# Performance work log

Hardware: AMD Instinct MI355X
Metric: run time of the kernel (lower is better)

The kernel has to match this reference:

```python
import jax, jax.numpy as jnp
import numpy as np

N_NODES = 100000
N_EDGES = 1600000
D = 64
BN_EPS = 1e-5


def setup_inputs() -> dict:
    key = jax.random.key(0)
    ks = jax.random.split(key, 10)
    s = 1.0 / np.sqrt(D)
    return {
        "features": jax.random.normal(ks[0], (N_NODES, D), dtype=jnp.float32),
        "src": jax.random.randint(ks[1], (N_EDGES,), 0, N_NODES, dtype=jnp.int32),
        "dst": jax.random.randint(ks[2], (N_EDGES,), 0, N_NODES, dtype=jnp.int32),
        "eps": jnp.zeros((), dtype=jnp.float32),
        "W1": jax.random.uniform(ks[3], (D, D), jnp.float32, -s, s),
        "b1": jax.random.uniform(ks[4], (D,), jnp.float32, -s, s),
        "W2": jax.random.uniform(ks[5], (D, D), jnp.float32, -s, s),
        "b2": jax.random.uniform(ks[6], (D,), jnp.float32, -s, s),
        "gamma": jnp.ones((D,), dtype=jnp.float32),
        "beta": jnp.zeros((D,), dtype=jnp.float32),
    }


def reference(features, src, dst, eps, W1, b1, W2, b2, gamma, beta):
    h_in = features
    # message passing: gather src node features, scatter-sum to dst (fn.copy_u + fn.sum)
    neigh = jax.ops.segment_sum(features[src], dst, num_segments=N_NODES)  # [N, D]
    # eps-weighted self term
    h = (1.0 + eps) * features + neigh
    # apply_func MLP: Linear -> ReLU -> Linear
    h = jnp.maximum(h @ W1 + b1, 0.0) @ W2 + b2
    # BatchNorm1d over nodes (training-mode batch statistics)
    mean = jnp.mean(h, axis=0)
    var = jnp.var(h, axis=0)
    h = (h - mean) * jax.lax.rsqrt(var + BN_EPS) * gamma + beta
    # activation
    h = jnp.maximum(h, 0.0)
    # residual (indim == outdim)
    h = h_in + h
    # dropout p=0 -> identity
    return h
```

## Files before the change

### kernel.cpp

```cpp
#include <hip/hip_runtime.h>
#include <hip/hip_fp16.h>

#define N_NODES 100000
#define N_EDGES 1600000
#define D 64
#define BN_EPS 1e-5f
#define NSHARD 8

#define NBKT 256
#define NPB 391
#define BKT_CAP 8192
#define NBBLK 391
#define SORT_T 1024

typedef _Float16 half8 __attribute__((ext_vector_type(8)));
typedef float f32x4 __attribute__((ext_vector_type(4)));

__global__ __launch_bounds__(256) void prep_k(
    const int* __restrict__ src, const int* __restrict__ dst,
    int* __restrict__ bkt_cnt, int* __restrict__ bktbuf,
    const float* __restrict__ feat, __half* __restrict__ feat16,
    const float* __restrict__ W1, const float* __restrict__ W2,
    _Float16* __restrict__ w1t, _Float16* __restrict__ w2t)
{
    __shared__ int h[NBKT], base[NBKT], cur[NBKT];
    const int blk = blockIdx.x;
    const int t = threadIdx.x;

    if (blk < NBBLK) {
        h[t] = 0; cur[t] = 0;
        __syncthreads();
        const int e0 = blk * 4096;
        int pk[16], b[16];
        #pragma unroll
        for (int i = 0; i < 16; ++i) {
            int e = e0 + i * 256 + t;
            if (e < N_EDGES) {
                int d = dst[e];
                b[i] = d / NPB;
                pk[i] = (src[e] << 9) | (d - b[i] * NPB);
                atomicAdd(&h[b[i]], 1);
            } else {
                b[i] = -1;
            }
        }
        __syncthreads();
        base[t] = atomicAdd(&bkt_cnt[t], h[t]);
        __syncthreads();
        #pragma unroll
        for (int i = 0; i < 16; ++i) {
            if (b[i] >= 0) {
                int p = atomicAdd(&cur[b[i]], 1);
                bktbuf[(size_t)b[i] * BKT_CAP + base[b[i]] + p] = pk[i];
            }
        }
    } else if (blk < NBBLK + 3125) {
        size_t i = ((size_t)(blk - NBBLK) * 256 + t) * 8;
        if (i < (size_t)N_NODES * D) {
            float4 v0 = *(const float4*)(feat + i);
            float4 v1 = *(const float4*)(feat + i + 4);
            __half2 o[4];
            o[0] = __floats2half2_rn(v0.x, v0.y);
            o[1] = __floats2half2_rn(v0.z, v0.w);
            o[2] = __floats2half2_rn(v1.x, v1.y);
            o[3] = __floats2half2_rn(v1.z, v1.w);
            *(float4*)(feat16 + i) = *(float4*)o;
        }
    } else {
        const int n = t >> 2;
        const int k0 = (t & 3) * 16;
        _Float16 o1[16], o2[16];
        #pragma unroll
        for (int j = 0; j < 16; ++j) {
            o1[j] = (_Float16)W1[(k0 + j) * 64 + n];
            o2[j] = (_Float16)W2[(k0 + j) * 64 + n];
        }
        #pragma unroll
        for (int j = 0; j < 16; j += 8) {
            *(half8*)(w1t + n * 64 + k0 + j) = *(half8*)&o1[j];
            *(half8*)(w2t + n * 64 + k0 + j) = *(half8*)&o2[j];
        }
    }
}

__global__ __launch_bounds__(SORT_T) void sortp_k(
    const int* __restrict__ bktbuf, const int* __restrict__ bkt_cnt,
    int* __restrict__ rowptr, int* __restrict__ col)
{
    __shared__ int h[NPB];
    __shared__ int cur[NPB];
    __shared__ int part[SORT_T];
    __shared__ int bsc[NBKT];

    const int b = blockIdx.x;
    const int t = threadIdx.x;
    const int nb0 = b * NPB;
    const int nodes_in = min(NPB, N_NODES - nb0);
    const int cnt = min(bkt_cnt[b], BKT_CAP);
    const int* buf = bktbuf + (size_t)b * BKT_CAP;

    if (t < NBKT) bsc[t] = min(bkt_cnt[t], BKT_CAP);
    __syncthreads();
    for (int off = 1; off < NBKT; off <<= 1) {
        int x = 0;
        if (t < NBKT) {
            x = bsc[t];
            if (t >= off) x += bsc[t - off];
        }
        __syncthreads();
        if (t < NBKT) bsc[t] = x;
        __syncthreads();
    }
    const int gbase = bsc[b] - cnt;

    if (t < NPB) h[t] = 0;
    __syncthreads();

    for (int i = t; i < cnt; i += SORT_T)
        atomicAdd(&h[buf[i] & 511], 1);
    __syncthreads();

    int a = (t < NPB) ? h[t] : 0;
    part[t] = a;
    __syncthreads();
    for (int off = 1; off < SORT_T; off <<= 1) {
        int x = part[t];
        int u = (t >= off) ? part[t - off] : 0;
        __syncthreads();
        part[t] = x + u;
        __syncthreads();
    }
    int excl = part[t] - a;
    if (t < NPB) {
        cur[t] = excl;
        if (t < nodes_in) rowptr[nb0 + t] = gbase + excl;
    }
    if (b == NBKT - 1 && t == 0) rowptr[N_NODES] = N_EDGES;
    __syncthreads();

    for (int i = t; i < cnt; i += SORT_T) {
        int pk = buf[i];
        int slot = atomicAdd(&cur[pk & 511], 1);
        col[gbase + slot] = pk >> 9;
    }
}

__device__ __forceinline__ void acc16(float* a, float4 r0, float4 r1)
{
    const __half2* h0 = (const __half2*)&r0;
    const __half2* h1 = (const __half2*)&r1;
    #pragma unroll
    for (int i = 0; i < 4; ++i) {
        float2 f = __half22float2(h0[i]);
        a[2 * i]     += f.x;
        a[2 * i + 1] += f.y;
    }
    #pragma unroll
    for (int i = 0; i < 4; ++i) {
        float2 f = __half22float2(h1[i]);
        a[8 + 2 * i]     += f.x;
        a[8 + 2 * i + 1] += f.y;
    }
}

__global__ __launch_bounds__(256) void gmlp_k(
    const __half* __restrict__ feat16, const int* __restrict__ rowptr,
    const int* __restrict__ col, const float* __restrict__ epsp,
    const _Float16* __restrict__ w1t, const _Float16* __restrict__ w2t,
    const float* __restrict__ b1, const float* __restrict__ b2,
    __half* __restrict__ h216, float* __restrict__ stats)
{
    __shared__ __align__(16) _Float16 xts[64 * 72];

    const int t    = threadIdx.x;
    const int lane = t & 63;
    const int nb   = blockIdx.x * 64;

    {
        const int nl   = t >> 2;
        const int node = nb + nl;
        const int c    = (t & 3) << 4;
        __half2 o[8];

        if (node < N_NODES) {
            const int lo = rowptr[node];
            const int hi = rowptr[node + 1];
            float a[16];
            #pragma unroll
            for (int i = 0; i < 16; ++i) a[i] = 0.f;

            int e = lo;
            for (; e + 3 < hi; e += 4) {
                const int s0 = col[e], s1 = col[e + 1], s2 = col[e + 2], s3 = col[e + 3];
                const __half* p0 = feat16 + (size_t)s0 * 64 + c;
                const __half* p1 = feat16 + (size_t)s1 * 64 + c;
                const __half* p2 = feat16 + (size_t)s2 * 64 + c;
                const __half* p3 = feat16 + (size_t)s3 * 64 + c;
                float4 r00 = *(const float4*)(p0), r01 = *(const float4*)(p0 + 8);
                float4 r10 = *(const float4*)(p1), r11 = *(const float4*)(p1 + 8);
                float4 r20 = *(const float4*)(p2), r21 = *(const float4*)(p2 + 8);
                float4 r30 = *(const float4*)(p3), r31 = *(const float4*)(p3 + 8);
                acc16(a, r00, r01);
                acc16(a, r10, r11);
                acc16(a, r20, r21);
                acc16(a, r30, r31);
            }
            for (; e < hi; ++e) {
                const __half* p = feat16 + (size_t)col[e] * 64 + c;
                float4 r0 = *(const float4*)(p), r1 = *(const float4*)(p + 8);
                acc16(a, r0, r1);
            }

            const float epsv = 1.0f + epsp[0];
            const size_t gb = (size_t)node * 64 + c;
            float4 s0 = *(const float4*)(feat16 + gb);
            float4 s1 = *(const float4*)(feat16 + gb + 8);
            const __half2* h0 = (const __half2*)&s0;
            const __half2* h1 = (const __half2*)&s1;
            #pragma unroll
            for (int i = 0; i < 4; ++i) {
                float2 f = __half22float2(h0[i]);
                o[i] = __floats2half2_rn(fmaf(epsv, f.x, a[2 * i]),
                                         fmaf(epsv, f.y, a[2 * i + 1]));
            }
            #pragma unroll
            for (int i = 0; i < 4; ++i) {
                float2 f = __half22float2(h1[i]);
                o[4 + i] = __floats2half2_rn(fmaf(epsv, f.x, a[8 + 2 * i]),
                                             fmaf(epsv, f.y, a[8 + 2 * i + 1]));
            }
        } else {
            #pragma unroll
            for (int i = 0; i < 8; ++i) o[i] = __floats2half2_rn(0.f, 0.f);
        }
        *(float4*)&xts[nl * 72 + c]     = *(float4*)&o[0];
        *(float4*)&xts[nl * 72 + c + 8] = *(float4*)&o[4];
    }
    asm volatile("s_waitcnt lgkmcnt(0)" ::: "memory");
    __builtin_amdgcn_sched_barrier(0);

    const int w     = t >> 6;
    const int m     = lane & 15;
    const int q     = lane >> 4;
    const int rbase = w * 16;

    const _Float16* xa = &xts[(rbase + m) * 72 + q * 8];
    half8 a0 = *(const half8*)(xa);
    half8 a1 = *(const half8*)(xa + 32);

    f32x4 acc[4];
    #pragma unroll
    for (int jt = 0; jt < 4; ++jt) {
        const float bias = b1[jt * 16 + m];
        acc[jt] = (f32x4){bias, bias, bias, bias};
        const _Float16* bw = w1t + (jt * 16 + m) * 64 + q * 8;
        half8 bf0 = *(const half8*)(bw);
        half8 bf1 = *(const half8*)(bw + 32);
        acc[jt] = __builtin_amdgcn_mfma_f32_16x16x32_f16(a0, bf0, acc[jt], 0, 0, 0);
        acc[jt] = __builtin_amdgcn_mfma_f32_16x16x32_f16(a1, bf1, acc[jt], 0, 0, 0);
    }

    #pragma unroll
    for (int jt = 0; jt < 4; ++jt)
        #pragma unroll
        for (int r = 0; r < 4; ++r)
            xts[(rbase + q * 4 + r) * 72 + jt * 16 + m] =
                (_Float16)fmaxf(acc[jt][r], 0.0f);
    asm volatile("s_waitcnt lgkmcnt(0)" ::: "memory");
    __builtin_amdgcn_sched_barrier(0);

    const _Float16* xw = &xts[(rbase + m) * 72 + q * 8];
    half8 c0 = *(const half8*)(xw);
    half8 c1 = *(const half8*)(xw + 32);

    f32x4 acc2[4];
    #pragma unroll
    for (int jt = 0; jt < 4; ++jt) {
        const float bias = b2[jt * 16 + m];
        acc2[jt] = (f32x4){bias, bias, bias, bias};
        const _Float16* bw = w2t + (jt * 16 + m) * 64 + q * 8;
        half8 bf0 = *(const half8*)(bw);
        half8 bf1 = *(const half8*)(bw + 32);
        acc2[jt] = __builtin_amdgcn_mfma_f32_16x16x32_f16(c0, bf0, acc2[jt], 0, 0, 0);
        acc2[jt] = __builtin_amdgcn_mfma_f32_16x16x32_f16(c1, bf1, acc2[jt], 0, 0, 0);
    }
    asm volatile("s_waitcnt lgkmcnt(0)" ::: "memory");
    __builtin_amdgcn_sched_barrier(0);

    float psums[4], psqs[4];
    #pragma unroll
    for (int jt = 0; jt < 4; ++jt) {
        float ps = 0.f, pq = 0.f;
        #pragma unroll
        for (int r = 0; r < 4; ++r) {
            const int row = rbase + q * 4 + r;
            const float v = acc2[jt][r];
            const float vv = (nb + row < N_NODES) ? v : 0.f;
            ps += vv;
            pq += vv * vv;
            xts[row * 72 + jt * 16 + m] = (_Float16)v;
        }
        ps += __shfl_xor(ps, 16, 64); ps += __shfl_xor(ps, 32, 64);
        pq += __shfl_xor(pq, 16, 64); pq += __shfl_xor(pq, 32, 64);
        psums[jt] = ps; psqs[jt] = pq;
    }
    if (lane < 16) {
        float* sp = stats + (size_t)(blockIdx.x & (NSHARD - 1)) * 128;
        #pragma unroll
        for (int jt = 0; jt < 4; ++jt) {
            unsafeAtomicAdd(sp + jt * 16 + lane,      psums[jt]);
            unsafeAtomicAdd(sp + 64 + jt * 16 + lane, psqs[jt]);
        }
    }
    asm volatile("s_waitcnt lgkmcnt(0)" ::: "memory");
    __builtin_amdgcn_sched_barrier(0);

    {
        const int rr = lane >> 2;
        const int cc = (lane & 3) * 16;
        const int gn = nb + rbase + rr;
        if (gn < N_NODES) {
            float4 r0 = *(const float4*)&xts[(rbase + rr) * 72 + cc];
            float4 r1 = *(const float4*)&xts[(rbase + rr) * 72 + cc + 8];
            *(float4*)(h216 + (size_t)gn * 64 + cc)     = r0;
            *(float4*)(h216 + (size_t)gn * 64 + cc + 8) = r1;
        }
    }
}

__global__ __launch_bounds__(256) void finish16_k(
    const float* __restrict__ feat, const __half* __restrict__ h216,
    const float* __restrict__ stats, const float* __restrict__ gamma,
    const float* __restrict__ beta, float* __restrict__ out)
{
    __shared__ float scs[64], shs[64];
    const int t = threadIdx.x;
    if (t < 64) {
        float s = 0.f, q = 0.f;
        #pragma unroll
        for (int c = 0; c < NSHARD; ++c) {
            s += stats[c * 128 + t];
            q += stats[c * 128 + 64 + t];
        }
        const float invN = 1.0f / (float)N_NODES;
        const float mean = s * invN;
        const float var  = q * invN - mean * mean;
        const float scale = gamma[t] * rsqrtf(var + BN_EPS);
        scs[t] = scale;
        shs[t] = beta[t] - mean * scale;
    }
    __syncthreads();
    size_t i = (size_t)blockIdx.x * 256 + t;
    if (i < (size_t)N_NODES * D / 4) {
        int j = (int)((i * 4) & 63);
        const __half2* hp = (const __half2*)(h216 + i * 4);
        float2 h0 = __half22float2(hp[0]);
        float2 h1 = __half22float2(hp[1]);
        float4 f = *(const float4*)(feat + i * 4);
        float4 o;
        o.x = fmaxf(fmaf(h0.x, scs[j + 0], shs[j + 0]), 0.f) + f.x;
        o.y = fmaxf(fmaf(h0.y, scs[j + 1], shs[j + 1]), 0.f) + f.y;
        o.z = fmaxf(fmaf(h1.x, scs[j + 2], shs[j + 2]), 0.f) + f.z;
        o.w = fmaxf(fmaf(h1.y, scs[j + 3], shs[j + 3]), 0.f) + f.w;
        *(float4*)(out + i * 4) = o;
    }
}

#define OCAP 7680

__global__ void bnstats_k(const float* __restrict__ stats,
                          const float* __restrict__ gamma,
                          const float* __restrict__ beta,
                          float* __restrict__ sf)
{
    int j = threadIdx.x;
    float s = 0.f, q = 0.f;
    for (int c = 0; c < NSHARD; ++c) {
        s += stats[c * 128 + j];
        q += stats[c * 128 + 64 + j];
    }
    const float invN = 1.0f / (float)N_NODES;
    float mean  = s * invN;
    float var   = q * invN - mean * mean;
    float scale = gamma[j] * rsqrtf(var + BN_EPS);
    sf[j]      = scale;
    sf[64 + j] = beta[j] - mean * scale;
}

__global__ __launch_bounds__(256) void bucket2_k(
    const int* __restrict__ src, const int* __restrict__ dst,
    int* __restrict__ bkt_cnt, int2* __restrict__ bktbuf)
{
    __shared__ int h[NBKT], base[NBKT], cur[NBKT];
    const int t = threadIdx.x;
    h[t] = 0; cur[t] = 0;
    __syncthreads();
    const int e0 = blockIdx.x * 4096;
    int s[16], d[16], b[16];
    #pragma unroll
    for (int i = 0; i < 16; ++i) {
        int e = e0 + i * 256 + t;
        if (e < N_EDGES) {
            s[i] = src[e];
            d[i] = dst[e];
            b[i] = d[i] / NPB;
            atomicAdd(&h[b[i]], 1);
        } else {
            b[i] = -1;
        }
    }
    __syncthreads();
    base[t] = atomicAdd(&bkt_cnt[t], h[t]);
    __syncthreads();
    #pragma unroll
    for (int i = 0; i < 16; ++i) {
        if (b[i] >= 0) {
            int p = atomicAdd(&cur[b[i]], 1);
            bktbuf[(size_t)b[i] * OCAP + base[b[i]] + p] = make_int2(s[i], d[i]);
        }
    }
}

__global__ __launch_bounds__(SORT_T) void sort2_k(
    const int2* __restrict__ bktbuf, const int* __restrict__ bkt_cnt,
    int* __restrict__ rowptr, int* __restrict__ col)
{
    __shared__ int h[NPB];
    __shared__ int cur[NPB];
    __shared__ int part[SORT_T];
    __shared__ int bsc[NBKT];

    const int b = blockIdx.x;
    const int t = threadIdx.x;
    const int nb0 = b * NPB;
    const int nodes_in = min(NPB, N_NODES - nb0);
    const int cnt = bkt_cnt[b];
    const int2* buf = bktbuf + (size_t)b * OCAP;

    if (t < NBKT) bsc[t] = bkt_cnt[t];
    __syncthreads();
    for (int off = 1; off < NBKT; off <<= 1) {
        int x = 0;
        if (t < NBKT) {
            x = bsc[t];
            if (t >= off) x += bsc[t - off];
        }
        __syncthreads();
        if (t < NBKT) bsc[t] = x;
        __syncthreads();
    }
    const int gbase = bsc[b] - cnt;

    if (t < NPB) h[t] = 0;
    __syncthreads();

    for (int i = t; i < cnt; i += SORT_T)
        atomicAdd(&h[buf[i].y - nb0], 1);
    __syncthreads();

    int a = (t < NPB) ? h[t] : 0;
    part[t] = a;
    __syncthreads();
    for (int off = 1; off < SORT_T; off <<= 1) {
        int x = part[t];
        int u = (t >= off) ? part[t - off] : 0;
        __syncthreads();
        part[t] = x + u;
        __syncthreads();
    }
    int excl = part[t] - a;
    if (t < NPB) {
        cur[t] = excl;
        if (t < nodes_in) rowptr[nb0 + t] = gbase + excl;
    }
    if (b == NBKT - 1 && t == 0) rowptr[N_NODES] = N_EDGES;
    __syncthreads();

    for (int i = t; i < cnt; i += SORT_T) {
        int2 r = buf[i];
        int slot = atomicAdd(&cur[r.y - nb0], 1);
        col[gbase + slot] = r.x;
    }
}

__global__ __launch_bounds__(256) void gather32_k(
    const float* __restrict__ feat, const int* __restrict__ rowptr,
    const int* __restrict__ col, const float* __restrict__ epsp,
    float* __restrict__ x)
{
    int node = blockIdx.x * 4 + (threadIdx.x >> 6);
    int lane = threadIdx.x & 63;
    if (node >= N_NODES) return;
    int g = lane >> 4;
    int c = (lane & 15) << 2;
    int lo = rowptr[node];
    int hi = rowptr[node + 1];
    float ax = 0.f, ay = 0.f, az = 0.f, aw = 0.f;
    int e = lo + g;
    for (; e + 4 < hi; e += 8) {
        int s0 = col[e];
        int s1 = col[e + 4];
        float4 v0 = *(const float4*)(feat + (size_t)s0 * D + c);
        float4 v1 = *(const float4*)(feat + (size_t)s1 * D + c);
        ax += v0.x; ay += v0.y; az += v0.z; aw += v0.w;
        ax += v1.x; ay += v1.y; az += v1.z; aw += v1.w;
    }
    if (e < hi) {
        float4 v = *(const float4*)(feat + (size_t)col[e] * D + c);
        ax += v.x; ay += v.y; az += v.z; aw += v.w;
    }
    #pragma unroll
    for (int off = 16; off <= 32; off <<= 1) {
        ax += __shfl_xor(ax, off, 64);
        ay += __shfl_xor(ay, off, 64);
        az += __shfl_xor(az, off, 64);
        aw += __shfl_xor(aw, off, 64);
    }
    if (g == 0) {
        float4 f = *(const float4*)(feat + (size_t)node * D + c);
        const float epsv = 1.0f + epsp[0];
        float4 r;
        r.x = fmaf(epsv, f.x, ax);
        r.y = fmaf(epsv, f.y, ay);
        r.z = fmaf(epsv, f.z, az);
        r.w = fmaf(epsv, f.w, aw);
        *(float4*)(x + (size_t)node * D + c) = r;
    }
}

__global__ __launch_bounds__(256) void mlp32_k(
    const float* __restrict__ x,
    const float* __restrict__ W1, const float* __restrict__ b1,
    const float* __restrict__ W2, const float* __restrict__ b2,
    float* __restrict__ h2out, float* __restrict__ stats)
{
    __shared__ float W1s[64 * 68];
    __shared__ float W2s[64 * 68];
    __shared__ float xs[64 * 65];
    __shared__ float b1s[64], b2s[64];

    const int t  = threadIdx.x;
    const int nb = blockIdx.x * 64;

    #pragma unroll
    for (int i = 0; i < 4; ++i) {
        int l  = t + i * 256;
        int k  = l >> 4;
        int j4 = (l & 15) << 2;
        *(float4*)(&W1s[k * 68 + j4]) = *(const float4*)(W1 + k * 64 + j4);
        *(float4*)(&W2s[k * 68 + j4]) = *(const float4*)(W2 + k * 64 + j4);
    }
    if (t < 64)       b1s[t]      = b1[t];
    else if (t < 128) b2s[t - 64] = b2[t - 64];

    #pragma unroll
    for (int i = 0; i < 2; ++i) {
        int n  = (t >> 3) + i * 32;
        int k8 = (t & 7) << 3;
        int gn = nb + n;
        float4 a = make_float4(0.f, 0.f, 0.f, 0.f), b = a;
        if (gn < N_NODES) {
            a = *(const float4*)(x + (size_t)gn * D + k8);
            b = *(const float4*)(x + (size_t)gn * D + k8 + 4);
        }
        *(float4*)&xs[n * 65 + k8]     = a;
        *(float4*)&xs[n * 65 + k8 + 4] = b;
    }
    __syncthreads();

    const int n0 = (t & 15) << 2;
    const int j0 = (t >> 4) << 2;
    const float* xr0 = &xs[(n0 + 0) * 65];
    const float* xr1 = &xs[(n0 + 1) * 65];
    const float* xr2 = &xs[(n0 + 2) * 65];
    const float* xr3 = &xs[(n0 + 3) * 65];

    float acc[4][4];
    #pragma unroll
    for (int a = 0; a < 4; ++a)
        #pragma unroll
        for (int b = 0; b < 4; ++b)
            acc[a][b] = b1s[j0 + b];

    #pragma unroll 8
    for (int k = 0; k < 64; ++k) {
        const float4 w = *(const float4*)(&W1s[k * 68 + j0]);
        const float x0 = xr0[k], x1 = xr1[k], x2 = xr2[k], x3 = xr3[k];
        acc[0][0] = fmaf(x0, w.x, acc[0][0]); acc[0][1] = fmaf(x0, w.y, acc[0][1]);
        acc[0][2] = fmaf(x0, w.z, acc[0][2]); acc[0][3] = fmaf(x0, w.w, acc[0][3]);
        acc[1][0] = fmaf(x1, w.x, acc[1][0]); acc[1][1] = fmaf(x1, w.y, acc[1][1]);
        acc[1][2] = fmaf(x1, w.z, acc[1][2]); acc[1][3] = fmaf(x1, w.w, acc[1][3]);
        acc[2][0] = fmaf(x2, w.x, acc[2][0]); acc[2][1] = fmaf(x2, w.y, acc[2][1]);
        acc[2][2] = fmaf(x2, w.z, acc[2][2]); acc[2][3] = fmaf(x2, w.w, acc[2][3]);
        acc[3][0] = fmaf(x3, w.x, acc[3][0]); acc[3][1] = fmaf(x3, w.y, acc[3][1]);
        acc[3][2] = fmaf(x3, w.z, acc[3][2]); acc[3][3] = fmaf(x3, w.w, acc[3][3]);
    }

    __syncthreads();
    #pragma unroll
    for (int a = 0; a < 4; ++a)
        #pragma unroll
        for (int b = 0; b < 4; ++b)
            xs[(n0 + a) * 65 + j0 + b] = fmaxf(acc[a][b], 0.0f);
    __syncthreads();

    float acc2[4][4];
    #pragma unroll
    for (int a = 0; a < 4; ++a)
        #pragma unroll
        for (int b = 0; b < 4; ++b)
            acc2[a][b] = b2s[j0 + b];

    #pragma unroll 8
    for (int k = 0; k < 64; ++k) {
        const float4 w = *(const float4*)(&W2s[k * 68 + j0]);
        const float x0 = xr0[k], x1 = xr1[k], x2 = xr2[k], x3 = xr3[k];
        acc2[0][0] = fmaf(x0, w.x, acc2[0][0]); acc2[0][1] = fmaf(x0, w.y, acc2[0][1]);
        acc2[0][2] = fmaf(x0, w.z, acc2[0][2]); acc2[0][3] = fmaf(x0, w.w, acc2[0][3]);
        acc2[1][0] = fmaf(x1, w.x, acc2[1][0]); acc2[1][1] = fmaf(x1, w.y, acc2[1][1]);
        acc2[1][2] = fmaf(x1, w.z, acc2[1][2]); acc2[1][3] = fmaf(x1, w.w, acc2[1][3]);
        acc2[2][0] = fmaf(x2, w.x, acc2[2][0]); acc2[2][1] = fmaf(x2, w.y, acc2[2][1]);
        acc2[2][2] = fmaf(x2, w.z, acc2[2][2]); acc2[2][3] = fmaf(x2, w.w, acc2[2][3]);
        acc2[3][0] = fmaf(x3, w.x, acc2[3][0]); acc2[3][1] = fmaf(x3, w.y, acc2[3][1]);
        acc2[3][2] = fmaf(x3, w.z, acc2[3][2]); acc2[3][3] = fmaf(x3, w.w, acc2[3][3]);
    }

    float psum[4] = {0.f, 0.f, 0.f, 0.f};
    float psq[4]  = {0.f, 0.f, 0.f, 0.f};
    #pragma unroll
    for (int a = 0; a < 4; ++a) {
        int gn = nb + n0 + a;
        if (gn < N_NODES) {
            float4 hh;
            hh.x = acc2[a][0]; hh.y = acc2[a][1]; hh.z = acc2[a][2]; hh.w = acc2[a][3];
            *(float4*)(h2out + (size_t)gn * 64 + j0) = hh;
            psum[0] += hh.x; psq[0] += hh.x * hh.x;
            psum[1] += hh.y; psq[1] += hh.y * hh.y;
            psum[2] += hh.z; psq[2] += hh.z * hh.z;
            psum[3] += hh.w; psq[3] += hh.w * hh.w;
        }
    }
    #pragma unroll
    for (int off = 8; off >= 1; off >>= 1)
        #pragma unroll
        for (int b = 0; b < 4; ++b) {
            psum[b] += __shfl_down(psum[b], off, 16);
            psq[b]  += __shfl_down(psq[b],  off, 16);
        }
    if ((t & 15) == 0) {
        float* sp = stats + (size_t)(blockIdx.x & (NSHARD - 1)) * 128;
        #pragma unroll
        for (int b = 0; b < 4; ++b) {
            unsafeAtomicAdd(sp + j0 + b,      psum[b]);
            unsafeAtomicAdd(sp + 64 + j0 + b, psq[b]);
        }
    }
}

__global__ __launch_bounds__(256) void finish_k(
    const float* __restrict__ feat, const float* __restrict__ sf,
    float* __restrict__ out)
{
    __shared__ float scs[64], shs[64];
    if (threadIdx.x < 64) {
        scs[threadIdx.x] = sf[threadIdx.x];
        shs[threadIdx.x] = sf[64 + threadIdx.x];
    }
    __syncthreads();
    size_t i = (size_t)blockIdx.x * 256 + threadIdx.x;
    if (i < (size_t)N_NODES * D / 4) {
        int j = (int)((i * 4) & 63);
        float4 h = *(float4*)(out + i * 4);
        float4 f = *(const float4*)(feat + i * 4);
        h.x = fmaxf(fmaf(h.x, scs[j + 0], shs[j + 0]), 0.f) + f.x;
        h.y = fmaxf(fmaf(h.y, scs[j + 1], shs[j + 1]), 0.f) + f.y;
        h.z = fmaxf(fmaf(h.z, scs[j + 2], shs[j + 2]), 0.f) + f.z;
        h.w = fmaxf(fmaf(h.w, scs[j + 3], shs[j + 3]), 0.f) + f.w;
        *(float4*)(out + i * 4) = h;
    }
}

extern "C" void kernel_launch(void* const* d_in, const int* in_sizes, int n_in,
                              void* d_out, int out_size, void* d_ws, size_t ws_size,
                              hipStream_t stream)
{
    const float* feat  = (const float*)d_in[0];
    const int*   src   = (const int*)d_in[1];
    const int*   dst   = (const int*)d_in[2];
    const float* eps   = (const float*)d_in[3];
    const float* W1    = (const float*)d_in[4];
    const float* b1    = (const float*)d_in[5];
    const float* W2    = (const float*)d_in[6];
    const float* b2    = (const float*)d_in[7];
    const float* gamma = (const float*)d_in[8];
    const float* beta  = (const float*)d_in[9];
    float* out = (float*)d_out;

    const size_t BKTSZ  = (size_t)NBKT * BKT_CAP * sizeof(int);
    const size_t F16SZ  = (size_t)N_NODES * D * sizeof(__half);
    const size_t COLSZ  = (size_t)N_EDGES * sizeof(int);
    const size_t RPSZ   = ((size_t)(N_NODES + 1) * sizeof(int) + 15) & ~(size_t)15;
    const size_t STATSZ = (size_t)NSHARD * 128 * sizeof(float);
    const size_t CNTSZ  = (size_t)NBKT * sizeof(int);
    const size_t TAIL   = STATSZ + CNTSZ + 128 * 4 + 2 * 4096 * sizeof(_Float16) + 256;
    const size_t need   = BKTSZ + 2 * F16SZ + COLSZ + RPSZ + TAIL;

    if (ws_size >= need) {
        char* p = (char*)d_ws;
        int*    bktbuf  = (int*)p;
        __half* h216    = (__half*)p;
        __half* feat16  = (__half*)(p + BKTSZ + F16SZ);
        int*    col     = (int*)(p + BKTSZ + 2 * F16SZ);
        int*    rowptr  = (int*)(p + BKTSZ + 2 * F16SZ + COLSZ);
        float*  stats   = (float*)(p + BKTSZ + 2 * F16SZ + COLSZ + RPSZ);
        int*    bkt_cnt = (int*)(stats + NSHARD * 128);
        float*  sf      = (float*)(bkt_cnt + NBKT);
        _Float16* w1t   = (_Float16*)(sf + 128);
        _Float16* w2t   = w1t + 4096;
        (void)sf;

        hipMemsetAsync(stats, 0, STATSZ + CNTSZ, stream);
        prep_k<<<NBBLK + 3125 + 1, 256, 0, stream>>>(src, dst, bkt_cnt, bktbuf,
                                                     feat, feat16, W1, W2, w1t, w2t);
        sortp_k<<<NBKT, SORT_T, 0, stream>>>(bktbuf, bkt_cnt, rowptr, col);
        gmlp_k<<<(N_NODES + 63) / 64, 256, 0, stream>>>(feat16, rowptr, col, eps,
                                                        w1t, w2t, b1, b2, h216, stats);
        finish16_k<<<(N_NODES * D / 4 + 255) / 256, 256, 0, stream>>>(
            feat, h216, stats, gamma, beta, out);
    } else {
        const size_t X32SZ = (size_t)N_NODES * D * sizeof(float);
        char* p = (char*)d_ws;
        float* x32    = (float*)p;
        int2*  bktbuf = (int2*)p;
        int*   col    = (int*)(p + X32SZ);
        int*   rowptr = col + N_EDGES;
        float* stats  = (float*)(rowptr + N_NODES + 1);
        int*   bkt_cnt = (int*)(stats + NSHARD * 128);
        float* sf     = (float*)(bkt_cnt + NBKT);

        hipMemsetAsync(stats, 0, STATSZ + NBKT * 4, stream);
        bucket2_k<<<(N_EDGES + 4095) / 4096, 256, 0, stream>>>(src, dst, bkt_cnt, bktbuf);
        sort2_k<<<NBKT, SORT_T, 0, stream>>>(bktbuf, bkt_cnt, rowptr, col);
        gather32_k<<<(N_NODES + 3) / 4, 256, 0, stream>>>(feat, rowptr, col, eps, x32);
        mlp32_k<<<(N_NODES + 63) / 64, 256, 0, stream>>>(x32, W1, b1, W2, b2, out, stats);
        bnstats_k<<<1, 64, 0, stream>>>(stats, gamma, beta, sf);
        finish_k<<<(N_NODES * D / 4 + 255) / 256, 256, 0, stream>>>(feat, sf, out);
    }
}
```

Before: 202.4 us.

## Shrink gather-MLP blocks to one wave and use wave-shuffle scans in sort

The fused gather+MLP kernel now uses 64-thread blocks of 16 nodes instead of 256-thread blocks of 64 nodes. This gives finer-grained scheduling and smaller shared-memory tiles, and it drops the bounds checks because 100000 divides evenly by 16. The bucket sort kernel replaces its shared-memory Hillis-Steele scans with wave shuffle reductions and scans, which cuts barrier rounds. The stats zeroing moves from the memset into the sort kernel. More blocks also means more atomic adds on the stats shards.

New measurement: 284.9 us. +40.8%, slower.

```diff
diff --git a/kernel.cpp b/kernel.cpp
--- a/kernel.cpp
+++ b/kernel.cpp
@@ -83,57 +83,63 @@
     }
 }
 
+__device__ __forceinline__ int wscan_incl(int x, int lane)
+{
+    #pragma unroll
+    for (int off = 1; off < 64; off <<= 1) {
+        int v = __shfl_up(x, off, 64);
+        if (lane >= off) x += v;
+    }
+    return x;
+}
+
 __global__ __launch_bounds__(SORT_T) void sortp_k(
     const int* __restrict__ bktbuf, const int* __restrict__ bkt_cnt,
-    int* __restrict__ rowptr, int* __restrict__ col)
+    int* __restrict__ rowptr, int* __restrict__ col, float* __restrict__ stats)
 {
     __shared__ int h[NPB];
     __shared__ int cur[NPB];
-    __shared__ int part[SORT_T];
-    __shared__ int bsc[NBKT];
-
-    const int b = blockIdx.x;
-    const int t = threadIdx.x;
-    const int nb0 = b * NPB;
+    __shared__ int wsum[16];
+
+    const int b    = blockIdx.x;
+    const int t    = threadIdx.x;
+    const int lane = t & 63;
+    const int wv   = t >> 6;
+    const int nb0  = b * NPB;
     const int nodes_in = min(NPB, N_NODES - nb0);
     const int cnt = min(bkt_cnt[b], BKT_CAP);
     const int* buf = bktbuf + (size_t)b * BKT_CAP;
 
-    if (t < NBKT) bsc[t] = min(bkt_cnt[t], BKT_CAP);
-    __syncthreads();
-    for (int off = 1; off < NBKT; off <<= 1) {
-        int x = 0;
-        if (t < NBKT) {
-            x = bsc[t];
-            if (t >= off) x += bsc[t - off];
-        }
-        __syncthreads();
-        if (t < NBKT) bsc[t] = x;
-        __syncthreads();
-    }
-    const int gbase = bsc[b] - cnt;
-
+    if (b == 0) stats[t] = 0.f;
+
+    int ci = 0;
+    if (t < NBKT && t < b) ci = min(bkt_cnt[t], BKT_CAP);
+    #pragma unroll
+    for (int off = 32; off >= 1; off >>= 1) ci += __shfl_xor(ci, off, 64);
+    if (lane == 0) wsum[wv] = ci;
     if (t < NPB) h[t] = 0;
     __syncthreads();
+    const int gbase = wsum[0] + wsum[1] + wsum[2] + wsum[3];
 
     for (int i = t; i < cnt; i += SORT_T)
         atomicAdd(&h[buf[i] & 511], 1);
     __syncthreads();
 
-    int a = (t < NPB) ? h[t] : 0;
-    part[t] = a;
-    __syncthreads();
-    for (int off = 1; off < SORT_T; off <<= 1) {
-        int x = part[t];
-        int u = (t >= off) ? part[t - off] : 0;
-        __syncthreads();
-        part[t] = x + u;
-        __syncthreads();
-    }
-    int excl = part[t] - a;
-    if (t < NPB) {
-        cur[t] = excl;
-        if (t < nodes_in) rowptr[nb0 + t] = gbase + excl;
+    int a = 0, x = 0;
+    if (wv < 7) {
+        a = (t < NPB) ? h[t] : 0;
+        x = wscan_incl(a, lane);
+        if (lane == 63) wsum[wv] = x;
+    }
+    __syncthreads();
+    if (wv < 7) {
+        int offs = 0;
+        for (int i = 0; i < wv; ++i) offs += wsum[i];
+        const int excl = x - a + offs;
+        if (t < NPB) {
+            cur[t] = excl;
+            if (t < nodes_in) rowptr[nb0 + t] = gbase + excl;
+        }
     }
     if (b == NBKT - 1 && t == 0) rowptr[N_NODES] = N_EDGES;
     __syncthreads();
@@ -163,75 +169,68 @@
     }
 }
 
-__global__ __launch_bounds__(256) void gmlp_k(
+__global__ __launch_bounds__(64, 8) void gmlp_k(
     const __half* __restrict__ feat16, const int* __restrict__ rowptr,
     const int* __restrict__ col, const float* __restrict__ epsp,
     const _Float16* __restrict__ w1t, const _Float16* __restrict__ w2t,
     const float* __restrict__ b1, const float* __restrict__ b2,
     __half* __restrict__ h216, float* __restrict__ stats)
 {
-    __shared__ __align__(16) _Float16 xts[64 * 72];
-
-    const int t    = threadIdx.x;
-    const int lane = t & 63;
-    const int nb   = blockIdx.x * 64;
+    __shared__ __align__(16) _Float16 xts[16 * 72];
+
+    const int t  = threadIdx.x;
+    const int nb = blockIdx.x * 16;
 
     {
         const int nl   = t >> 2;
         const int node = nb + nl;
         const int c    = (t & 3) << 4;
+        const int lo = rowptr[node];
+        const int hi = rowptr[node + 1];
+        float a[16];
+        #pragma unroll
+        for (int i = 0; i < 16; ++i) a[i] = 0.f;
+
+        int e = lo;
+        for (; e + 3 < hi; e += 4) {
+            const int s0 = col[e], s1 = col[e + 1], s2 = col[e + 2], s3 = col[e + 3];
+            const __half* p0 = feat16 + (size_t)s0 * 64 + c;
+            const __half* p1 = feat16 + (size_t)s1 * 64 + c;
+            const __half* p2 = feat16 + (size_t)s2 * 64 + c;
+            const __half* p3 = feat16 + (size_t)s3 * 64 + c;
+            float4 r00 = *(const float4*)(p0), r01 = *(const float4*)(p0 + 8);
+            float4 r10 = *(const float4*)(p1), r11 = *(const float4*)(p1 + 8);
+            float4 r20 = *(const float4*)(p2), r21 = *(const float4*)(p2 + 8);
+            float4 r30 = *(const float4*)(p3), r31 = *(const float4*)(p3 + 8);
+            acc16(a, r00, r01);
+            acc16(a, r10, r11);
+            acc16(a, r20, r21);
+            acc16(a, r30, r31);
+        }
+        for (; e < hi; ++e) {
+            const __half* p = feat16 + (size_t)col[e] * 64 + c;
+            float4 r0 = *(const float4*)(p), r1 = *(const float4*)(p + 8);
+            acc16(a, r0, r1);
+        }
+
+        const float epsv = 1.0f + epsp[0];
+        const size_t gb = (size_t)node * 64 + c;
+        float4 s0 = *(const float4*)(feat16 + gb);
+        float4 s1 = *(const float4*)(feat16 + gb + 8);
+        const __half2* h0 = (const __half2*)&s0;
+        const __half2* h1 = (const __half2*)&s1;
         __half2 o[8];
-
-        if (node < N_NODES) {
-            const int lo = rowptr[node];
-            const int hi = rowptr[node + 1];
-            float a[16];
-            #pragma unroll
-            for (int i = 0; i < 16; ++i) a[i] = 0.f;
-
-            int e = lo;
-            for (; e + 3 < hi; e += 4) {
-                const int s0 = col[e], s1 = col[e + 1], s2 = col[e + 2], s3 = col[e + 3];
-                const __half* p0 = feat16 + (size_t)s0 * 64 + c;
-                const __half* p1 = feat16 + (size_t)s1 * 64 + c;
-                const __half* p2 = feat16 + (size_t)s2 * 64 + c;
-                const __half* p3 = feat16 + (size_t)s3 * 64 + c;
-                float4 r00 = *(const float4*)(p0), r01 = *(const float4*)(p0 + 8);
-                float4 r10 = *(const float4*)(p1), r11 = *(const float4*)(p1 + 8);
-                float4 r20 = *(const float4*)(p2), r21 = *(const float4*)(p2 + 8);
-                float4 r30 = *(const float4*)(p3), r31 = *(const float4*)(p3 + 8);
-                acc16(a, r00, r01);
-                acc16(a, r10, r11);
-                acc16(a, r20, r21);
-                acc16(a, r30, r31);
-            }
-            for (; e < hi; ++e) {
-                const __half* p = feat16 + (size_t)col[e] * 64 + c;
-                float4 r0 = *(const float4*)(p), r1 = *(const float4*)(p + 8);
-                acc16(a, r0, r1);
-            }
-
-            const float epsv = 1.0f + epsp[0];
-            const size_t gb = (size_t)node * 64 + c;
-            float4 s0 = *(const float4*)(feat16 + gb);
-            float4 s1 = *(const float4*)(feat16 + gb + 8);
-            const __half2* h0 = (const __half2*)&s0;
-            const __half2* h1 = (const __half2*)&s1;
-            #pragma unroll
-            for (int i = 0; i < 4; ++i) {
-                float2 f = __half22float2(h0[i]);
-                o[i] = __floats2half2_rn(fmaf(epsv, f.x, a[2 * i]),
-                                         fmaf(epsv, f.y, a[2 * i + 1]));
-            }
-            #pragma unroll
-            for (int i = 0; i < 4; ++i) {
-                float2 f = __half22float2(h1[i]);
-                o[4 + i] = __floats2half2_rn(fmaf(epsv, f.x, a[8 + 2 * i]),
-                                             fmaf(epsv, f.y, a[8 + 2 * i + 1]));
-            }
-        } else {
-            #pragma unroll
-            for (int i = 0; i < 8; ++i) o[i] = __floats2half2_rn(0.f, 0.f);
+        #pragma unroll
+        for (int i = 0; i < 4; ++i) {
+            float2 f = __half22float2(h0[i]);
+            o[i] = __floats2half2_rn(fmaf(epsv, f.x, a[2 * i]),
+                                     fmaf(epsv, f.y, a[2 * i + 1]));
+        }
+        #pragma unroll
+        for (int i = 0; i < 4; ++i) {
+            float2 f = __half22float2(h1[i]);
+            o[4 + i] = __floats2half2_rn(fmaf(epsv, f.x, a[8 + 2 * i]),
+                                         fmaf(epsv, f.y, a[8 + 2 * i + 1]));
         }
         *(float4*)&xts[nl * 72 + c]     = *(float4*)&o[0];
         *(float4*)&xts[nl * 72 + c + 8] = *(float4*)&o[4];
@@ -239,12 +238,10 @@
     asm volatile("s_waitcnt lgkmcnt(0)" ::: "memory");
     __builtin_amdgcn_sched_barrier(0);
 
-    const int w     = t >> 6;
-    const int m     = lane & 15;
-    const int q     = lane >> 4;
-    const int rbase = w * 16;
-
-    const _Float16* xa = &xts[(rbase + m) * 72 + q * 8];
+    const int m = t & 15;
+    const int q = t >> 4;
+
+    const _Float16* xa = &xts[m * 72 + q * 8];
     half8 a0 = *(const half8*)(xa);
     half8 a1 = *(const half8*)(xa + 32);
 
@@ -264,12 +261,12 @@
     for (int jt = 0; jt < 4; ++jt)
         #pragma unroll
         for (int r = 0; r < 4; ++r)
-            xts[(rbase + q * 4 + r) * 72 + jt * 16 + m] =
+            xts[(q * 4 + r) * 72 + jt * 16 + m] =
                 (_Float16)fmaxf(acc[jt][r], 0.0f);
     asm volatile("s_waitcnt lgkmcnt(0)" ::: "memory");
     __builtin_amdgcn_sched_barrier(0);
 
-    const _Float16* xw = &xts[(rbase + m) * 72 + q * 8];
+    const _Float16* xw = &xts[m * 72 + q * 8];
     half8 c0 = *(const half8*)(xw);
     half8 c1 = *(const half8*)(xw + 32);
 
@@ -293,38 +290,35 @@
         float ps = 0.f, pq = 0.f;
         #pragma unroll
         for (int r = 0; r < 4; ++r) {
-            const int row = rbase + q * 4 + r;
+            const int row = q * 4 + r;
             const float v = acc2[jt][r];
-            const float vv = (nb + row < N_NODES) ? v : 0.f;
-            ps += vv;
-            pq += vv * vv;
+            ps += v;
+            pq += v * v;
             xts[row * 72 + jt * 16 + m] = (_Float16)v;
         }
         ps += __shfl_xor(ps, 16, 64); ps += __shfl_xor(ps, 32, 64);
         pq += __shfl_xor(pq, 16, 64); pq += __shfl_xor(pq, 32, 64);
         psums[jt] = ps; psqs[jt] = pq;
     }
-    if (lane < 16) {
+    if (t < 16) {
         float* sp = stats + (size_t)(blockIdx.x & (NSHARD - 1)) * 128;
         #pragma unroll
         for (int jt = 0; jt < 4; ++jt) {
-            unsafeAtomicAdd(sp + jt * 16 + lane,      psums[jt]);
-            unsafeAtomicAdd(sp + 64 + jt * 16 + lane, psqs[jt]);
+            unsafeAtomicAdd(sp + jt * 16 + t,      psums[jt]);
+            unsafeAtomicAdd(sp + 64 + jt * 16 + t, psqs[jt]);
         }
     }
     asm volatile("s_waitcnt lgkmcnt(0)" ::: "memory");
     __builtin_amdgcn_sched_barrier(0);
 
     {
-        const int rr = lane >> 2;
-        const int cc = (lane & 3) * 16;
-        const int gn = nb + rbase + rr;
-        if (gn < N_NODES) {
-            float4 r0 = *(const float4*)&xts[(rbase + rr) * 72 + cc];
-            float4 r1 = *(const float4*)&xts[(rbase + rr) * 72 + cc + 8];
-            *(float4*)(h216 + (size_t)gn * 64 + cc)     = r0;
-            *(float4*)(h216 + (size_t)gn * 64 + cc + 8) = r1;
-        }
+        const int rr = t >> 2;
+        const int cc = (t & 3) * 16;
+        const int gn = nb + rr;
+        float4 r0 = *(const float4*)&xts[rr * 72 + cc];
+        float4 r1 = *(const float4*)&xts[rr * 72 + cc + 8];
+        *(float4*)(h216 + (size_t)gn * 64 + cc)     = r0;
+        *(float4*)(h216 + (size_t)gn * 64 + cc + 8) = r1;
     }
 }
 
@@ -719,12 +713,12 @@
         _Float16* w2t   = w1t + 4096;
         (void)sf;
 
-        hipMemsetAsync(stats, 0, STATSZ + CNTSZ, stream);
+        hipMemsetAsync(bkt_cnt, 0, CNTSZ, stream);
         prep_k<<<NBBLK + 3125 + 1, 256, 0, stream>>>(src, dst, bkt_cnt, bktbuf,
                                                      feat, feat16, W1, W2, w1t, w2t);
-        sortp_k<<<NBKT, SORT_T, 0, stream>>>(bktbuf, bkt_cnt, rowptr, col);
-        gmlp_k<<<(N_NODES + 63) / 64, 256, 0, stream>>>(feat16, rowptr, col, eps,
-                                                        w1t, w2t, b1, b2, h216, stats);
+        sortp_k<<<NBKT, SORT_T, 0, stream>>>(bktbuf, bkt_cnt, rowptr, col, stats);
+        gmlp_k<<<N_NODES / 16, 64, 0, stream>>>(feat16, rowptr, col, eps,
+                                                w1t, w2t, b1, b2, h216, stats);
         finish16_k<<<(N_NODES * D / 4 + 255) / 256, 256, 0, stream>>>(
             feat, h216, stats, gamma, beta, out);
     } else {
```
